# Optimization experiments

Measured on AMD Instinct MI355X. Metric: run time of the kernel, lower is better.

The kernel has to match this reference:

```python
import jax, jax.numpy as jnp
import numpy as np

H = 16          # num_heads
W = 256         # attention_window
D_MODEL = 1024
D_FF = 4096
EPS = 1e-5


def _layernorm(x, g, b):
    mu = jnp.mean(x, axis=-1, keepdims=True)
    var = jnp.mean(jnp.square(x - mu), axis=-1, keepdims=True)
    return (x - mu) * jax.lax.rsqrt(var + EPS) * g + b


def _sliding_attn(q, k, v, w):
    # q,k,v: [B,H,S,d]; each query attends to keys in [i-w, i+w]
    B, Hh, S, d = q.shape
    nc = S // w
    qc = q.reshape(B, Hh, nc, w, d)
    kp = jnp.pad(k, ((0, 0), (0, 0), (w, w), (0, 0)))
    vp = jnp.pad(v, ((0, 0), (0, 0), (w, w), (0, 0)))
    # gather 3w keys per chunk (prev w, current w, next w)
    idx = (jnp.arange(nc) * w)[:, None] + jnp.arange(3 * w)[None, :]  # [nc, 3w]
    kc = kp[:, :, idx, :]  # [B,H,nc,3w,d]
    vc = vp[:, :, idx, :]
    scores = jnp.einsum('bhcqd,bhckd->bhcqk', qc, kc)  # [B,H,nc,w,3w]
    q_pos = jnp.arange(nc)[:, None, None] * w + jnp.arange(w)[None, :, None]
    k_pos = jnp.arange(nc)[:, None, None] * w - w + jnp.arange(3 * w)[None, None, :]
    rel = k_pos - q_pos
    valid = (jnp.abs(rel) <= w) & (k_pos >= 0) & (k_pos < S)  # [nc,w,3w]
    scores = jnp.where(valid[None, None], scores, jnp.float32(-1e9))
    p = jax.nn.softmax(scores, axis=-1)
    out = jnp.einsum('bhcqk,bhckd->bhcqd', p, vc)
    return out.reshape(B, Hh, S, d)


def setup_inputs() -> dict:
    key = jax.random.key(0)
    ks = jax.random.split(key, 8)
    B, S = 2, 4096
    src = jax.random.normal(ks[0], (B, S, D_MODEL), dtype=jnp.float32)
    ln1_g = jnp.ones((D_MODEL,), jnp.float32)
    ln1_b = jnp.zeros((D_MODEL,), jnp.float32)
    ln2_g = jnp.ones((D_MODEL,), jnp.float32)
    ln2_b = jnp.zeros((D_MODEL,), jnp.float32)
    W1 = jax.random.normal(ks[1], (D_MODEL, D_FF), jnp.float32) * 0.02
    b1 = jnp.zeros((D_FF,), jnp.float32)
    W2 = jax.random.normal(ks[2], (D_FF, D_MODEL), jnp.float32) * 0.02
    b2 = jnp.zeros((D_MODEL,), jnp.float32)
    return {"src": src, "ln1_g": ln1_g, "ln1_b": ln1_b, "ln2_g": ln2_g,
            "ln2_b": ln2_b, "W1": W1, "b1": b1, "W2": W2, "b2": b2}


def reference(src, ln1_g, ln1_b, ln2_g, ln2_b, W1, b1, W2, b2):
    B, S, _ = src.shape
    d_head = D_MODEL // H
    qkv = src.reshape(B, S, H, d_head).transpose(0, 2, 1, 3)  # [B,H,S,d]
    attn = _sliding_attn(qkv, qkv, qkv, W)
    attn = attn.transpose(0, 2, 1, 3).reshape(B, S, D_MODEL)
    x = _layernorm(src + attn, ln1_g, ln1_b)
    ff = jnp.maximum(x @ W1 + b1, 0.0) @ W2 + b2
    return _layernorm(x + ff, ln2_g, ln2_b)
```

## Files before the change

### kernel.cpp

```cpp
#include <hip/hip_runtime.h>

typedef __bf16 bf16x8 __attribute__((ext_vector_type(8)));
typedef __bf16 bf16x4 __attribute__((ext_vector_type(4)));
typedef float f32x4 __attribute__((ext_vector_type(4)));

#define MFMA16(a, b, c) __builtin_amdgcn_mfma_f32_16x16x32_bf16((a), (b), (c), 0, 0, 0)

__device__ __forceinline__ void gload_lds16(const void* g, void* l) {
  __builtin_amdgcn_global_load_lds(
      (const __attribute__((address_space(1))) unsigned int*)g,
      (__attribute__((address_space(3))) unsigned int*)l, 16, 0, 0);
}

__global__ __launch_bounds__(256, 2) void attn_kernel(const float* __restrict__ src,
                                                      __bf16* __restrict__ attn_out) {
  const int bid = blockIdx.x;
  const int half = bid & 1;
  const int c = (bid >> 1) & 15;
  const int h = (bid >> 5) & 15;
  const int b = bid >> 9;
  const int tid = threadIdx.x;
  const int w = tid >> 6;
  const int lane = tid & 63;
  const int lg = lane >> 4;
  const int l16 = lane & 15;
  const size_t b4096 = (size_t)b * 4096;

  __shared__ __bf16 Ks[2][64][72];
  __shared__ __bf16 Vt[2][64][72];

  const int q0 = c * 256 + half * 128 + w * 32;
  const float LOG2E = 1.44269504f;

  bf16x8 qf[2][2];
#pragma unroll
  for (int qfi = 0; qfi < 2; ++qfi)
#pragma unroll
    for (int ks = 0; ks < 2; ++ks) {
      const int row = q0 + qfi * 16 + l16;
      const int d0 = ks * 32 + lg * 8;
      const float* p = src + (b4096 + row) * 1024 + h * 64 + d0;
      bf16x8 v;
#pragma unroll
      for (int j = 0; j < 8; ++j) v[j] = (__bf16)(p[j] * LOG2E);
      qf[qfi][ks] = v;
    }

  int krow[4];
#pragma unroll
  for (int kf = 0; kf < 4; ++kf)
    krow[kf] = ((kf >> 1) << 5) + ((l16 >> 2) << 3) + ((kf & 1) << 2) + (l16 & 3);

  const f32x4 z4 = {0.f, 0.f, 0.f, 0.f};
  float m_run[2], l_run[2];
  f32x4 o[2][4];
#pragma unroll
  for (int qfi = 0; qfi < 2; ++qfi) {
    m_run[qfi] = -6.0e8f;
    l_run[qfi] = 0.f;
#pragma unroll
    for (int df = 0; df < 4; ++df) o[qfi][df] = z4;
  }

  const int stage_key = tid >> 2;
  const int d0a = (tid & 3) * 16;
  const int vcolA = stage_key ^ d0a;
  const int vcolB = stage_key ^ (d0a + 8);

  int kpos = c * 256 - 256 + stage_key;
  float4 g4[4];
  {
    const int rc = min(max(kpos, 0), 4095);
    const float* p = src + (b4096 + rc) * 1024 + h * 64 + d0a;
#pragma unroll
    for (int i = 0; i < 4; ++i) g4[i] = *(const float4*)(p + i * 4);
  }

  for (int kt = 0; kt < 12; ++kt) {
    const int kbase = c * 256 - 256 + kt * 64;
    const int cur = kt & 1;
    bf16x8 kvA, kvB;
    const bool inb = ((unsigned)kpos < 4096u);
    kvA[0] = (__bf16)(inb ? g4[0].x : 0.f); kvA[1] = (__bf16)(inb ? g4[0].y : 0.f);
    kvA[2] = (__bf16)(inb ? g4[0].z : 0.f); kvA[3] = (__bf16)(inb ? g4[0].w : 0.f);
    kvA[4] = (__bf16)(inb ? g4[1].x : 0.f); kvA[5] = (__bf16)(inb ? g4[1].y : 0.f);
    kvA[6] = (__bf16)(inb ? g4[1].z : 0.f); kvA[7] = (__bf16)(inb ? g4[1].w : 0.f);
    kvB[0] = (__bf16)(inb ? g4[2].x : 0.f); kvB[1] = (__bf16)(inb ? g4[2].y : 0.f);
    kvB[2] = (__bf16)(inb ? g4[2].z : 0.f); kvB[3] = (__bf16)(inb ? g4[2].w : 0.f);
    kvB[4] = (__bf16)(inb ? g4[3].x : 0.f); kvB[5] = (__bf16)(inb ? g4[3].y : 0.f);
    kvB[6] = (__bf16)(inb ? g4[3].z : 0.f); kvB[7] = (__bf16)(inb ? g4[3].w : 0.f);

    *(bf16x8*)&Ks[cur][stage_key][d0a] = kvA;
    *(bf16x8*)&Ks[cur][stage_key][d0a + 8] = kvB;
#pragma unroll
    for (int j = 0; j < 8; ++j) Vt[cur][d0a + j][vcolA] = kvA[j];
#pragma unroll
    for (int j = 0; j < 8; ++j) Vt[cur][d0a + 8 + j][vcolB] = kvB[j];
    asm volatile("s_waitcnt lgkmcnt(0)" ::: "memory");
    __builtin_amdgcn_s_barrier();
    __builtin_amdgcn_sched_barrier(0);

    kpos += 64;
    if (kt < 11) {
      const int rc = min(max(kpos, 0), 4095);
      const float* p = src + (b4096 + rc) * 1024 + h * 64 + d0a;
#pragma unroll
      for (int i = 0; i < 4; ++i) g4[i] = *(const float4*)(p + i * 4);
    }

    const bool skip = (kbase + 63 < 0) | (kbase >= 4096) |
                      (kbase + 63 < q0 - 256) | (kbase > q0 + 31 + 256);
    if (skip) continue;

    f32x4 s[4][2];
#pragma unroll
    for (int kf = 0; kf < 4; ++kf)
#pragma unroll
      for (int qfi = 0; qfi < 2; ++qfi) s[kf][qfi] = z4;

#pragma unroll
    for (int ks = 0; ks < 2; ++ks) {
      bf16x8 ka[4];
#pragma unroll
      for (int kf = 0; kf < 4; ++kf)
        ka[kf] = *(const bf16x8*)&Ks[cur][krow[kf]][ks * 32 + lg * 8];
#pragma unroll
      for (int kf = 0; kf < 4; ++kf)
#pragma unroll
        for (int qfi = 0; qfi < 2; ++qfi)
          s[kf][qfi] = MFMA16(ka[kf], qf[qfi][ks], s[kf][qfi]);
    }

    const bool needmask = (kbase < 0) | (kbase > 4032) |
                          (kbase < q0 - 225) | (kbase > q0 + 193);
    if (needmask) {
#pragma unroll
      for (int qfi = 0; qfi < 2; ++qfi) {
        const int qp = q0 + qfi * 16 + l16;
#pragma unroll
        for (int kf = 0; kf < 4; ++kf) {
          const int kb0 = kbase + ((kf >> 1) << 5) + 8 * lg + ((kf & 1) << 2);
#pragma unroll
          for (int reg = 0; reg < 4; ++reg) {
            const int kp = kb0 + reg;
            const int rel = kp - qp;
            if (rel > 256 || rel < -256 || kp < 0 || kp >= 4096)
              s[kf][qfi][reg] = -1e9f;
          }
        }
      }
    }

    bf16x4 pb[4][2];
#pragma unroll
    for (int qfi = 0; qfi < 2; ++qfi) {
      float tm = s[0][qfi][0];
#pragma unroll
      for (int kf = 0; kf < 4; ++kf)
#pragma unroll
        for (int reg = 0; reg < 4; ++reg) tm = fmaxf(tm, s[kf][qfi][reg]);
      tm = fmaxf(tm, __shfl_xor(tm, 16, 64));
      tm = fmaxf(tm, __shfl_xor(tm, 32, 64));

      const bool nomax = __all(tm <= m_run[qfi] + 8.f);
      float scl = 1.f;
      if (!nomax) {
        const float mn = fmaxf(m_run[qfi], tm);
        scl = exp2f(m_run[qfi] - mn);
        m_run[qfi] = mn;
#pragma unroll
        for (int df = 0; df < 4; ++df)
#pragma unroll
          for (int reg = 0; reg < 4; ++reg) o[qfi][df][reg] *= scl;
      }
      const float mn = m_run[qfi];

      float rs = 0.f;
#pragma unroll
      for (int kf = 0; kf < 4; ++kf) {
        bf16x4 pv;
#pragma unroll
        for (int reg = 0; reg < 4; ++reg) {
          const float p = exp2f(s[kf][qfi][reg] - mn);
          rs += p;
          pv[reg] = (__bf16)p;
        }
        pb[kf][qfi] = pv;
      }
      rs += __shfl_xor(rs, 16, 64);
      rs += __shfl_xor(rs, 32, 64);
      l_run[qfi] = l_run[qfi] * scl + rs;
    }

#pragma unroll
    for (int ks2 = 0; ks2 < 2; ++ks2) {
      bf16x8 av[4];
#pragma unroll
      for (int df = 0; df < 4; ++df) {
        const int d = df * 16 + l16;
        const int blk = (ks2 * 4 + lg) ^ (d >> 3);
        av[df] = *(const bf16x8*)&Vt[cur][d][blk * 8];
      }
#pragma unroll
      for (int qfi = 0; qfi < 2; ++qfi) {
        const bf16x8 bq = __builtin_shufflevector(pb[2 * ks2][qfi], pb[2 * ks2 + 1][qfi],
                                                  0, 1, 2, 3, 4, 5, 6, 7);
#pragma unroll
        for (int df = 0; df < 4; ++df)
          o[qfi][df] = MFMA16(av[df], bq, o[qfi][df]);
      }
    }
  }

#pragma unroll
  for (int qfi = 0; qfi < 2; ++qfi) {
    const float inv = 1.0f / l_run[qfi];
    const int qp = q0 + qfi * 16 + l16;
    __bf16* dst = attn_out + (b4096 + qp) * 1024 + h * 64 + lg * 4;
#pragma unroll
    for (int df = 0; df < 4; ++df) {
      bf16x4 y;
      y[0] = (__bf16)(o[qfi][df][0] * inv);
      y[1] = (__bf16)(o[qfi][df][1] * inv);
      y[2] = (__bf16)(o[qfi][df][2] * inv);
      y[3] = (__bf16)(o[qfi][df][3] * inv);
      *(bf16x4*)&dst[df * 16] = y;
    }
  }
}

template <int MODE>
__global__ __launch_bounds__(512, 2) void gemm8p(const __bf16* __restrict__ A,
                                                 const __bf16* __restrict__ Bt,
                                                 const float* __restrict__ bias,
                                                 __bf16* __restrict__ out,
                                                 size_t ksplit_stride,
                                                 int M, int N, int Kstride, int Klen) {
  __shared__ char smem[131072];
  const int tid = threadIdx.x;
  const int w = tid >> 6;
  const int lane = tid & 63;
  const int lg = lane >> 4;
  const int l16 = lane & 15;
  const int wr = w >> 2;
  const int wc = w & 3;

  const int nbn = N >> 8;
  const int x = ((int)blockIdx.x & 7) * ((int)gridDim.x >> 3) + ((int)blockIdx.x >> 3);
  const long bm = (long)(x / nbn) * 256;
  const long bn = (long)(x % nbn) * 256;
  const long koff = (long)blockIdx.y * Klen;
  out += (size_t)blockIdx.y * ksplit_stride;

  const f32x4 z4 = {0.f, 0.f, 0.f, 0.f};
  f32x4 acc[8][4];
#pragma unroll
  for (int i = 0; i < 8; ++i)
#pragma unroll
    for (int j = 0; j < 4; ++j) acc[i][j] = z4;

  const int srow = tid >> 2;
  const int g0 = (tid & 3) ^ ((tid >> 3) & 3);
  const __bf16* Ag = A + (size_t)(bm + srow) * Kstride + koff + g0 * 8;
  const __bf16* Bg = Bt + (size_t)(bn + srow) * Kstride + koff + g0 * 8;

  auto stage = [&](int kt, int osel, int isB, int khalf) {
    const __bf16* src = (isB ? Bg : Ag) + (size_t)kt * 64 + khalf * 32;
    char* dst = smem + (isB ? 65536 : 0) + osel * 32768 + khalf * 16384 + (w << 10);
    gload_lds16(src, dst);
    gload_lds16(src + (size_t)128 * Kstride, dst + 8192);
  };

  const int lslot = (lg ^ ((l16 >> 1) & 3)) << 4;
  const char* pA = smem + (wr * 128 + l16) * 64 + lslot;
  const char* pB = smem + 65536 + (wc * 64 + l16) * 64 + lslot;
  auto rdA = [&](int sel, int rf, int ks) {
    return *(const bf16x8*)(pA + sel * 32768 + ks * 16384 + rf * 1024);
  };
  auto rdB = [&](int sel, int cf, int ks) {
    return *(const bf16x8*)(pB + sel * 32768 + ks * 16384 + cf * 1024);
  };

  const int NT = Klen >> 6;

  stage(0, 0, 0, 0);
  stage(0, 0, 1, 0);
  stage(0, 0, 0, 1);
  stage(0, 0, 1, 1);
  asm volatile("s_waitcnt vmcnt(4)" ::: "memory");
  __builtin_amdgcn_s_barrier();
  __builtin_amdgcn_sched_barrier(0);

  for (int t = 0; t < NT; ++t) {
    const int sel = t & 1, osel = sel ^ 1;
    const bool st = (t + 1) < NT;
    bf16x8 af[8], bf[4];

#pragma unroll
    for (int rf = 0; rf < 8; ++rf) af[rf] = rdA(sel, rf, 0);
#pragma unroll
    for (int cf = 0; cf < 4; ++cf) bf[cf] = rdB(sel, cf, 0);
    if (st) { stage(t + 1, osel, 0, 0); stage(t + 1, osel, 1, 0); }
    __builtin_amdgcn_s_setprio(1);
#pragma unroll
    for (int rf = 0; rf < 8; ++rf)
#pragma unroll
      for (int cf = 0; cf < 4; ++cf)
        acc[rf][cf] = MFMA16(af[rf], bf[cf], acc[rf][cf]);
    __builtin_amdgcn_s_setprio(0);
    if (st) asm volatile("s_waitcnt vmcnt(4)" ::: "memory");
    else    asm volatile("s_waitcnt vmcnt(0)" ::: "memory");
    __builtin_amdgcn_s_barrier();
    __builtin_amdgcn_sched_barrier(0);

#pragma unroll
    for (int rf = 0; rf < 8; ++rf) af[rf] = rdA(sel, rf, 1);
#pragma unroll
    for (int cf = 0; cf < 4; ++cf) bf[cf] = rdB(sel, cf, 1);
    if (st) { stage(t + 1, osel, 0, 1); stage(t + 1, osel, 1, 1); }
    __builtin_amdgcn_s_setprio(1);
#pragma unroll
    for (int rf = 0; rf < 8; ++rf)
#pragma unroll
      for (int cf = 0; cf < 4; ++cf)
        acc[rf][cf] = MFMA16(af[rf], bf[cf], acc[rf][cf]);
    __builtin_amdgcn_s_setprio(0);
    if (st) asm volatile("s_waitcnt vmcnt(4)" ::: "memory");
    __builtin_amdgcn_s_barrier();
    __builtin_amdgcn_sched_barrier(0);
  }

  float bv[4];
  if (MODE == 0) {
#pragma unroll
    for (int cf = 0; cf < 4; ++cf) bv[cf] = bias[bn + wc * 64 + cf * 16 + l16];
  }
#pragma unroll
  for (int rf = 0; rf < 8; ++rf)
#pragma unroll
    for (int reg = 0; reg < 4; ++reg) {
      const long row = bm + wr * 128 + rf * 16 + lg * 4 + reg;
#pragma unroll
      for (int cf = 0; cf < 4; ++cf) {
        const long col = bn + wc * 64 + cf * 16 + l16;
        if (MODE == 0) {
          out[row * N + col] = (__bf16)fmaxf(acc[rf][cf][reg] + bv[cf], 0.f);
        } else {
          out[row * N + col] = (__bf16)acc[rf][cf][reg];
        }
      }
    }
}

__global__ __launch_bounds__(256) void transpose_cvt(const float* __restrict__ in,
                                                     __bf16* __restrict__ out,
                                                     int R, int C) {
  __shared__ float tile[64][65];
  const long r0 = (long)blockIdx.y * 64;
  const long c0 = (long)blockIdx.x * 64;
  const int t = threadIdx.x;
  const int tr = t >> 6;
  const int tc = t & 63;
#pragma unroll
  for (int i = 0; i < 16; ++i) {
    const int r = tr * 16 + i;
    tile[r][tc] = in[(r0 + r) * C + c0 + tc];
  }
  __syncthreads();
#pragma unroll
  for (int i = 0; i < 16; ++i) {
    const int cc = tr * 16 + i;
    out[(c0 + cc) * (long)R + r0 + tc] = (__bf16)tile[tc][cc];
  }
}

__global__ __launch_bounds__(256) void ln1_kernel(const float* __restrict__ src,
                                                  const __bf16* __restrict__ attn,
                                                  const float* __restrict__ g,
                                                  const float* __restrict__ bta,
                                                  __bf16* __restrict__ xb) {
  const long r = blockIdx.x;
  const int t = threadIdx.x;
  const float4 a = *(const float4*)&src[r * 1024 + t * 4];
  const bf16x4 cc = *(const bf16x4*)&attn[r * 1024 + t * 4];
  float v[4] = {a.x + (float)cc[0], a.y + (float)cc[1],
                a.z + (float)cc[2], a.w + (float)cc[3]};
  float s = v[0] + v[1] + v[2] + v[3];
  float s2 = v[0] * v[0] + v[1] * v[1] + v[2] * v[2] + v[3] * v[3];
#pragma unroll
  for (int off = 32; off >= 1; off >>= 1) {
    s += __shfl_xor(s, off, 64);
    s2 += __shfl_xor(s2, off, 64);
  }
  __shared__ float red[8];
  if ((t & 63) == 0) { red[t >> 6] = s; red[(t >> 6) + 4] = s2; }
  __syncthreads();
  s = red[0] + red[1] + red[2] + red[3];
  s2 = red[4] + red[5] + red[6] + red[7];
  const float mu = s * (1.f / 1024.f);
  const float var = s2 * (1.f / 1024.f) - mu * mu;
  const float rstd = rsqrtf(var + 1e-5f);
  const float4 gv = *(const float4*)&g[t * 4];
  const float4 bv = *(const float4*)&bta[t * 4];
  bf16x4 y;
  y[0] = (__bf16)((v[0] - mu) * rstd * gv.x + bv.x);
  y[1] = (__bf16)((v[1] - mu) * rstd * gv.y + bv.y);
  y[2] = (__bf16)((v[2] - mu) * rstd * gv.z + bv.z);
  y[3] = (__bf16)((v[3] - mu) * rstd * gv.w + bv.w);
  *(bf16x4*)&xb[r * 1024 + t * 4] = y;
}

__global__ __launch_bounds__(256) void ln2_kernel(const __bf16* __restrict__ xb,
                                                  const __bf16* __restrict__ f0,
                                                  const __bf16* __restrict__ f1,
                                                  const float* __restrict__ b2,
                                                  const float* __restrict__ g,
                                                  const float* __restrict__ bta,
                                                  float* __restrict__ out) {
  const long r = blockIdx.x;
  const int t = threadIdx.x;
  const bf16x4 xv = *(const bf16x4*)&xb[r * 1024 + t * 4];
  const bf16x4 f0v = *(const bf16x4*)&f0[r * 1024 + t * 4];
  const bf16x4 f1v = *(const bf16x4*)&f1[r * 1024 + t * 4];
  const float4 b2v = *(const float4*)&b2[t * 4];
  float v[4];
#pragma unroll
  for (int i = 0; i < 4; ++i)
    v[i] = (float)xv[i] + (float)f0v[i] + (float)f1v[i] +
           ((const float*)&b2v)[i];
  float s = v[0] + v[1] + v[2] + v[3];
  float s2 = v[0] * v[0] + v[1] * v[1] + v[2] * v[2] + v[3] * v[3];
#pragma unroll
  for (int off = 32; off >= 1; off >>= 1) {
    s += __shfl_xor(s, off, 64);
    s2 += __shfl_xor(s2, off, 64);
  }
  __shared__ float red[8];
  if ((t & 63) == 0) { red[t >> 6] = s; red[(t >> 6) + 4] = s2; }
  __syncthreads();
  s = red[0] + red[1] + red[2] + red[3];
  s2 = red[4] + red[5] + red[6] + red[7];
  const float mu = s * (1.f / 1024.f);
  const float var = s2 * (1.f / 1024.f) - mu * mu;
  const float rstd = rsqrtf(var + 1e-5f);
  const float4 gv = *(const float4*)&g[t * 4];
  const float4 bv = *(const float4*)&bta[t * 4];
  float4 y;
  y.x = (v[0] - mu) * rstd * gv.x + bv.x;
  y.y = (v[1] - mu) * rstd * gv.y + bv.y;
  y.z = (v[2] - mu) * rstd * gv.z + bv.z;
  y.w = (v[3] - mu) * rstd * gv.w + bv.w;
  *(float4*)&out[r * 1024 + t * 4] = y;
}

extern "C" void kernel_launch(void* const* d_in, const int* in_sizes, int n_in,
                              void* d_out, int out_size, void* d_ws, size_t ws_size,
                              hipStream_t stream) {
  const float* src = (const float*)d_in[0];
  const float* ln1_g = (const float*)d_in[1];
  const float* ln1_b = (const float*)d_in[2];
  const float* ln2_g = (const float*)d_in[3];
  const float* ln2_b = (const float*)d_in[4];
  const float* W1 = (const float*)d_in[5];
  const float* b1 = (const float*)d_in[6];
  const float* W2 = (const float*)d_in[7];
  const float* b2 = (const float*)d_in[8];
  float* out = (float*)d_out;
  char* ws = (char*)d_ws;

  const size_t MB = 1048576;
  __bf16* xb = (__bf16*)ws;
  __bf16* attn_b = (__bf16*)(ws + 16 * MB);
  __bf16* ffb = attn_b;
  __bf16* ff1b = (__bf16*)(ws + 32 * MB);
  __bf16* w1t = (__bf16*)(ws + 48 * MB);
  __bf16* w2t = (__bf16*)(ws + 56 * MB);
  __bf16* hbuf = (__bf16*)(ws + 64 * MB);

  int Mc = 8192;
  while (Mc > 512 && 64 * MB + (size_t)Mc * 8192 > ws_size) Mc >>= 1;

  transpose_cvt<<<dim3(4096 / 64, 1024 / 64), 256, 0, stream>>>(W1, w1t, 1024, 4096);
  transpose_cvt<<<dim3(1024 / 64, 4096 / 64), 256, 0, stream>>>(W2, w2t, 4096, 1024);
  attn_kernel<<<1024, 256, 0, stream>>>(src, attn_b);
  ln1_kernel<<<8192, 256, 0, stream>>>(src, attn_b, ln1_g, ln1_b, xb);
  for (int m0 = 0; m0 < 8192; m0 += Mc) {
    gemm8p<0><<<dim3((Mc / 256) * (4096 / 256), 1), 512, 0, stream>>>(
        xb + (size_t)m0 * 1024, w1t, b1, hbuf, 0, Mc, 4096, 1024, 1024);
    gemm8p<1><<<dim3((Mc / 256) * (1024 / 256), 2), 512, 0, stream>>>(
        hbuf, w2t, nullptr, ffb + (size_t)m0 * 1024, (size_t)8192 * 1024,
        Mc, 1024, 4096, 2048);
  }
  ln2_kernel<<<8192, 256, 0, stream>>>(xb, ffb, ff1b, b2, ln2_g, ln2_b, out);
}
```

Measured before the change: 242.1 us.

## Triple-buffer K/V LDS staging and overlap next-tile writes with compute

Moves the attention kernel's K/V staging from double to triple LDS buffering. The convert-and-store of tile kt+1 now happens between the QK MFMAs and the softmax/PV of tile kt, with the global load for kt+2 issued two tiles ahead. This leaves one barrier per iteration, and LDS stores and global latency overlap with compute instead of sitting in front of the barrier. In exchange, LDS use grows by half, which may limit occupancy at two blocks per CU, and register pressure rises.

```diff
diff --git a/kernel.cpp b/kernel.cpp
--- a/kernel.cpp
+++ b/kernel.cpp
@@ -11,6 +11,8 @@
       (const __attribute__((address_space(1))) unsigned int*)g,
       (__attribute__((address_space(3))) unsigned int*)l, 16, 0, 0);
 }
+
+struct G4 { float4 a, b, c, d; };
 
 __global__ __launch_bounds__(256, 2) void attn_kernel(const float* __restrict__ src,
                                                       __bf16* __restrict__ attn_out) {
@@ -26,8 +28,8 @@
   const int l16 = lane & 15;
   const size_t b4096 = (size_t)b * 4096;
 
-  __shared__ __bf16 Ks[2][64][72];
-  __shared__ __bf16 Vt[2][64][72];
+  __shared__ __bf16 Ks[3][64][72];
+  __shared__ __bf16 Vt[3][64][72];
 
   const int q0 = c * 256 + half * 128 + w * 32;
   const float LOG2E = 1.44269504f;
@@ -66,51 +68,53 @@
   const int d0a = (tid & 3) * 16;
   const int vcolA = stage_key ^ d0a;
   const int vcolB = stage_key ^ (d0a + 8);
-
-  int kpos = c * 256 - 256 + stage_key;
-  float4 g4[4];
-  {
-    const int rc = min(max(kpos, 0), 4095);
+  const int kb00 = c * 256 - 256;
+
+  auto issue = [&](int n) {
+    const int kp = kb00 + n * 64 + stage_key;
+    const int rc = min(max(kp, 0), 4095);
     const float* p = src + (b4096 + rc) * 1024 + h * 64 + d0a;
-#pragma unroll
-    for (int i = 0; i < 4; ++i) g4[i] = *(const float4*)(p + i * 4);
-  }
+    G4 r;
+    r.a = *(const float4*)(p + 0);
+    r.b = *(const float4*)(p + 4);
+    r.c = *(const float4*)(p + 8);
+    r.d = *(const float4*)(p + 12);
+    return r;
+  };
+  auto cw = [&](int n, const G4& g) {
+    const int kp = kb00 + n * 64 + stage_key;
+    const bool inb = ((unsigned)kp < 4096u);
+    bf16x8 kvA, kvB;
+    kvA[0] = (__bf16)(inb ? g.a.x : 0.f); kvA[1] = (__bf16)(inb ? g.a.y : 0.f);
+    kvA[2] = (__bf16)(inb ? g.a.z : 0.f); kvA[3] = (__bf16)(inb ? g.a.w : 0.f);
+    kvA[4] = (__bf16)(inb ? g.b.x : 0.f); kvA[5] = (__bf16)(inb ? g.b.y : 0.f);
+    kvA[6] = (__bf16)(inb ? g.b.z : 0.f); kvA[7] = (__bf16)(inb ? g.b.w : 0.f);
+    kvB[0] = (__bf16)(inb ? g.c.x : 0.f); kvB[1] = (__bf16)(inb ? g.c.y : 0.f);
+    kvB[2] = (__bf16)(inb ? g.c.z : 0.f); kvB[3] = (__bf16)(inb ? g.c.w : 0.f);
+    kvB[4] = (__bf16)(inb ? g.d.x : 0.f); kvB[5] = (__bf16)(inb ? g.d.y : 0.f);
+    kvB[6] = (__bf16)(inb ? g.d.z : 0.f); kvB[7] = (__bf16)(inb ? g.d.w : 0.f);
+    const int bsel = n % 3;
+    *(bf16x8*)&Ks[bsel][stage_key][d0a] = kvA;
+    *(bf16x8*)&Ks[bsel][stage_key][d0a + 8] = kvB;
+#pragma unroll
+    for (int j = 0; j < 8; ++j) Vt[bsel][d0a + j][vcolA] = kvA[j];
+#pragma unroll
+    for (int j = 0; j < 8; ++j) Vt[bsel][d0a + 8 + j][vcolB] = kvB[j];
+  };
+
+  G4 g = issue(0);
+  cw(0, g);
+  g = issue(1);
+  asm volatile("s_waitcnt lgkmcnt(0)" ::: "memory");
 
   for (int kt = 0; kt < 12; ++kt) {
-    const int kbase = c * 256 - 256 + kt * 64;
-    const int cur = kt & 1;
-    bf16x8 kvA, kvB;
-    const bool inb = ((unsigned)kpos < 4096u);
-    kvA[0] = (__bf16)(inb ? g4[0].x : 0.f); kvA[1] = (__bf16)(inb ? g4[0].y : 0.f);
-    kvA[2] = (__bf16)(inb ? g4[0].z : 0.f); kvA[3] = (__bf16)(inb ? g4[0].w : 0.f);
-    kvA[4] = (__bf16)(inb ? g4[1].x : 0.f); kvA[5] = (__bf16)(inb ? g4[1].y : 0.f);
-    kvA[6] = (__bf16)(inb ? g4[1].z : 0.f); kvA[7] = (__bf16)(inb ? g4[1].w : 0.f);
-    kvB[0] = (__bf16)(inb ? g4[2].x : 0.f); kvB[1] = (__bf16)(inb ? g4[2].y : 0.f);
-    kvB[2] = (__bf16)(inb ? g4[2].z : 0.f); kvB[3] = (__bf16)(inb ? g4[2].w : 0.f);
-    kvB[4] = (__bf16)(inb ? g4[3].x : 0.f); kvB[5] = (__bf16)(inb ? g4[3].y : 0.f);
-    kvB[6] = (__bf16)(inb ? g4[3].z : 0.f); kvB[7] = (__bf16)(inb ? g4[3].w : 0.f);
-
-    *(bf16x8*)&Ks[cur][stage_key][d0a] = kvA;
-    *(bf16x8*)&Ks[cur][stage_key][d0a + 8] = kvB;
-#pragma unroll
-    for (int j = 0; j < 8; ++j) Vt[cur][d0a + j][vcolA] = kvA[j];
-#pragma unroll
-    for (int j = 0; j < 8; ++j) Vt[cur][d0a + 8 + j][vcolB] = kvB[j];
-    asm volatile("s_waitcnt lgkmcnt(0)" ::: "memory");
+    const int kbase = kb00 + kt * 64;
+    const int cur = kt % 3;
     __builtin_amdgcn_s_barrier();
     __builtin_amdgcn_sched_barrier(0);
 
-    kpos += 64;
-    if (kt < 11) {
-      const int rc = min(max(kpos, 0), 4095);
-      const float* p = src + (b4096 + rc) * 1024 + h * 64 + d0a;
-#pragma unroll
-      for (int i = 0; i < 4; ++i) g4[i] = *(const float4*)(p + i * 4);
-    }
-
     const bool skip = (kbase + 63 < 0) | (kbase >= 4096) |
                       (kbase + 63 < q0 - 256) | (kbase > q0 + 31 + 256);
-    if (skip) continue;
 
     f32x4 s[4][2];
 #pragma unroll
@@ -118,98 +122,107 @@
 #pragma unroll
       for (int qfi = 0; qfi < 2; ++qfi) s[kf][qfi] = z4;
 
-#pragma unroll
-    for (int ks = 0; ks < 2; ++ks) {
-      bf16x8 ka[4];
-#pragma unroll
-      for (int kf = 0; kf < 4; ++kf)
-        ka[kf] = *(const bf16x8*)&Ks[cur][krow[kf]][ks * 32 + lg * 8];
-#pragma unroll
-      for (int kf = 0; kf < 4; ++kf)
-#pragma unroll
-        for (int qfi = 0; qfi < 2; ++qfi)
-          s[kf][qfi] = MFMA16(ka[kf], qf[qfi][ks], s[kf][qfi]);
+    if (!skip) {
+#pragma unroll
+      for (int ks = 0; ks < 2; ++ks) {
+        bf16x8 ka[4];
+#pragma unroll
+        for (int kf = 0; kf < 4; ++kf)
+          ka[kf] = *(const bf16x8*)&Ks[cur][krow[kf]][ks * 32 + lg * 8];
+#pragma unroll
+        for (int kf = 0; kf < 4; ++kf)
+#pragma unroll
+          for (int qfi = 0; qfi < 2; ++qfi)
+            s[kf][qfi] = MFMA16(ka[kf], qf[qfi][ks], s[kf][qfi]);
+      }
     }
 
-    const bool needmask = (kbase < 0) | (kbase > 4032) |
-                          (kbase < q0 - 225) | (kbase > q0 + 193);
-    if (needmask) {
-#pragma unroll
-      for (int qfi = 0; qfi < 2; ++qfi) {
-        const int qp = q0 + qfi * 16 + l16;
-#pragma unroll
-        for (int kf = 0; kf < 4; ++kf) {
-          const int kb0 = kbase + ((kf >> 1) << 5) + 8 * lg + ((kf & 1) << 2);
-#pragma unroll
-          for (int reg = 0; reg < 4; ++reg) {
-            const int kp = kb0 + reg;
-            const int rel = kp - qp;
-            if (rel > 256 || rel < -256 || kp < 0 || kp >= 4096)
-              s[kf][qfi][reg] = -1e9f;
+    if (kt + 1 < 12) cw(kt + 1, g);
+    if (kt + 2 < 12) g = issue(kt + 2);
+
+    if (!skip) {
+      const bool needmask = (kbase < 0) | (kbase > 4032) |
+                            (kbase < q0 - 225) | (kbase > q0 + 193);
+      if (needmask) {
+#pragma unroll
+        for (int qfi = 0; qfi < 2; ++qfi) {
+          const int qp = q0 + qfi * 16 + l16;
+#pragma unroll
+          for (int kf = 0; kf < 4; ++kf) {
+            const int kb0 = kbase + ((kf >> 1) << 5) + 8 * lg + ((kf & 1) << 2);
+#pragma unroll
+            for (int reg = 0; reg < 4; ++reg) {
+              const int kp = kb0 + reg;
+              const int rel = kp - qp;
+              if (rel > 256 || rel < -256 || kp < 0 || kp >= 4096)
+                s[kf][qfi][reg] = -1e9f;
+            }
           }
         }
       }
-    }
-
-    bf16x4 pb[4][2];
-#pragma unroll
-    for (int qfi = 0; qfi < 2; ++qfi) {
-      float tm = s[0][qfi][0];
-#pragma unroll
-      for (int kf = 0; kf < 4; ++kf)
-#pragma unroll
-        for (int reg = 0; reg < 4; ++reg) tm = fmaxf(tm, s[kf][qfi][reg]);
-      tm = fmaxf(tm, __shfl_xor(tm, 16, 64));
-      tm = fmaxf(tm, __shfl_xor(tm, 32, 64));
-
-      const bool nomax = __all(tm <= m_run[qfi] + 8.f);
-      float scl = 1.f;
-      if (!nomax) {
-        const float mn = fmaxf(m_run[qfi], tm);
-        scl = exp2f(m_run[qfi] - mn);
-        m_run[qfi] = mn;
-#pragma unroll
-        for (int df = 0; df < 4; ++df)
-#pragma unroll
-          for (int reg = 0; reg < 4; ++reg) o[qfi][df][reg] *= scl;
+
+      bf16x4 pb[4][2];
+#pragma unroll
+      for (int qfi = 0; qfi < 2; ++qfi) {
+        float tm = s[0][qfi][0];
+#pragma unroll
+        for (int kf = 0; kf < 4; ++kf)
+#pragma unroll
+          for (int reg = 0; reg < 4; ++reg) tm = fmaxf(tm, s[kf][qfi][reg]);
+        tm = fmaxf(tm, __shfl_xor(tm, 16, 64));
+        tm = fmaxf(tm, __shfl_xor(tm, 32, 64));
+
+        const bool nomax = __all(tm <= m_run[qfi] + 8.f);
+        float scl = 1.f;
+        if (!nomax) {
+          const float mn = fmaxf(m_run[qfi], tm);
+          scl = exp2f(m_run[qfi] - mn);
+          m_run[qfi] = mn;
+#pragma unroll
+          for (int df = 0; df < 4; ++df)
+#pragma unroll
+            for (int reg = 0; reg < 4; ++reg) o[qfi][df][reg] *= scl;
+        }
+        const float mn = m_run[qfi];
+
+        float rs = 0.f;
+#pragma unroll
+        for (int kf = 0; kf < 4; ++kf) {
+          bf16x4 pv;
+#pragma unroll
+          for (int reg = 0; reg < 4; ++reg) {
+            const float p = exp2f(s[kf][qfi][reg] - mn);
+            rs += p;
+            pv[reg] = (__bf16)p;
+          }
+          pb[kf][qfi] = pv;
+        }
+        rs += __shfl_xor(rs, 16, 64);
+        rs += __shfl_xor(rs, 32, 64);
+        l_run[qfi] = l_run[qfi] * scl + rs;
       }
-      const float mn = m_run[qfi];
-
-      float rs = 0.f;
-#pragma unroll
-      for (int kf = 0; kf < 4; ++kf) {
-        bf16x4 pv;
-#pragma unroll
-        for (int reg = 0; reg < 4; ++reg) {
-          const float p = exp2f(s[kf][qfi][reg] - mn);
-          rs += p;
-          pv[reg] = (__bf16)p;
+
+#pragma unroll
+      for (int ks2 = 0; ks2 < 2; ++ks2) {
+        bf16x8 av[4];
+#pragma unroll
+        for (int df = 0; df < 4; ++df) {
+          const int d = df * 16 + l16;
+          const int blk = (ks2 * 4 + lg) ^ (d >> 3);
+          av[df] = *(const bf16x8*)&Vt[cur][d][blk * 8];
         }
-        pb[kf][qfi] = pv;
-      }
-      rs += __shfl_xor(rs, 16, 64);
-      rs += __shfl_xor(rs, 32, 64);
-      l_run[qfi] = l_run[qfi] * scl + rs;
-    }
-
-#pragma unroll
-    for (int ks2 = 0; ks2 < 2; ++ks2) {
-      bf16x8 av[4];
-#pragma unroll
-      for (int df = 0; df < 4; ++df) {
-        const int d = df * 16 + l16;
-        const int blk = (ks2 * 4 + lg) ^ (d >> 3);
-        av[df] = *(const bf16x8*)&Vt[cur][d][blk * 8];
-      }
-#pragma unroll
-      for (int qfi = 0; qfi < 2; ++qfi) {
-        const bf16x8 bq = __builtin_shufflevector(pb[2 * ks2][qfi], pb[2 * ks2 + 1][qfi],
-                                                  0, 1, 2, 3, 4, 5, 6, 7);
-#pragma unroll
-        for (int df = 0; df < 4; ++df)
-          o[qfi][df] = MFMA16(av[df], bq, o[qfi][df]);
+#pragma unroll
+        for (int qfi = 0; qfi < 2; ++qfi) {
+          const bf16x8 bq = __builtin_shufflevector(pb[2 * ks2][qfi], pb[2 * ks2 + 1][qfi],
+                                                    0, 1, 2, 3, 4, 5, 6, 7);
+#pragma unroll
+          for (int df = 0; df < 4; ++df)
+            o[qfi][df] = MFMA16(av[df], bq, o[qfi][df]);
+        }
       }
     }
+
+    asm volatile("s_waitcnt lgkmcnt(0)" ::: "memory");
   }
 
 #pragma unroll
```

Measured after the change: 244.3 us. Within noise of the previous version (+0.9%).

## Restructure GEMM mainloop into quarter-tile phases with 128-byte swizzled LDS layout

Applied to the files above, without the earlier changes.

Reorganizes the GEMM main loop so each 64-wide K tile is split into four MFMA phases over half-tiles of A and B. Loads for the next tile are issued in quarters interleaved with those phases, so global-to-LDS traffic overlaps compute more finely. The LDS layout moves from two 32-column halves to full 64-column rows of 128 bytes with an XOR swizzle keyed on the row, to avoid bank conflicts. The cost is more barriers per tile and tighter buffer-reuse ordering, which risks races if the stage and barrier sequencing is wrong. It also assumes NT is even.

```diff
diff --git a/kernel.cpp b/kernel.cpp
--- a/kernel.cpp
+++ b/kernel.cpp
@@ -259,75 +259,130 @@
 #pragma unroll
     for (int j = 0; j < 4; ++j) acc[i][j] = z4;
 
-  const int srow = tid >> 2;
-  const int g0 = (tid & 3) ^ ((tid >> 3) & 3);
+  const int srow = tid >> 3;
+  const int g0 = (tid & 7) ^ (srow & 7);
   const __bf16* Ag = A + (size_t)(bm + srow) * Kstride + koff + g0 * 8;
   const __bf16* Bg = Bt + (size_t)(bn + srow) * Kstride + koff + g0 * 8;
-
-  auto stage = [&](int kt, int osel, int isB, int khalf) {
-    const __bf16* src = (isB ? Bg : Ag) + (size_t)kt * 64 + khalf * 32;
-    char* dst = smem + (isB ? 65536 : 0) + osel * 32768 + khalf * 16384 + (w << 10);
-    gload_lds16(src, dst);
-    gload_lds16(src + (size_t)128 * Kstride, dst + 8192);
+  char* ldst = smem + (w << 10);
+
+  auto stage = [&](int kt, int which) {
+    const __bf16* s = ((which & 2) ? Bg : Ag) +
+                      (size_t)((which & 1) * 128) * Kstride + (size_t)kt * 64;
+    char* d = ldst + ((kt & 1) << 16) + ((which & 2) << 14) + ((which & 1) << 14);
+    gload_lds16(s, d);
+    gload_lds16(s + (size_t)64 * Kstride, d + 8192);
   };
 
-  const int lslot = (lg ^ ((l16 >> 1) & 3)) << 4;
-  const char* pA = smem + (wr * 128 + l16) * 64 + lslot;
-  const char* pB = smem + 65536 + (wc * 64 + l16) * 64 + lslot;
+  const unsigned rsw = (unsigned)((l16 & 7) << 4);
+  const char* pA = smem + wr * 16384 + l16 * 128;
+  const char* pB = smem + 32768 + (wc >> 1) * 16384 + ((wc & 1) * 64 + l16) * 128;
   auto rdA = [&](int sel, int rf, int ks) {
-    return *(const bf16x8*)(pA + sel * 32768 + ks * 16384 + rf * 1024);
+    return *(const bf16x8*)(pA + (sel << 16) + rf * 2048 +
+                            ((unsigned)((ks << 6) | (lg << 4)) ^ rsw));
   };
   auto rdB = [&](int sel, int cf, int ks) {
-    return *(const bf16x8*)(pB + sel * 32768 + ks * 16384 + cf * 1024);
+    return *(const bf16x8*)(pB + (sel << 16) + cf * 2048 +
+                            ((unsigned)((ks << 6) | (lg << 4)) ^ rsw));
   };
 
   const int NT = Klen >> 6;
 
-  stage(0, 0, 0, 0);
-  stage(0, 0, 1, 0);
-  stage(0, 0, 0, 1);
-  stage(0, 0, 1, 1);
+  stage(0, 0); stage(0, 1); stage(0, 2); stage(0, 3);
+  stage(1, 2); stage(1, 3);
   asm volatile("s_waitcnt vmcnt(4)" ::: "memory");
   __builtin_amdgcn_s_barrier();
   __builtin_amdgcn_sched_barrier(0);
 
-  for (int t = 0; t < NT; ++t) {
-    const int sel = t & 1, osel = sel ^ 1;
-    const bool st = (t + 1) < NT;
-    bf16x8 af[8], bf[4];
-
-#pragma unroll
-    for (int rf = 0; rf < 8; ++rf) af[rf] = rdA(sel, rf, 0);
-#pragma unroll
-    for (int cf = 0; cf < 4; ++cf) bf[cf] = rdB(sel, cf, 0);
-    if (st) { stage(t + 1, osel, 0, 0); stage(t + 1, osel, 1, 0); }
-    __builtin_amdgcn_s_setprio(1);
-#pragma unroll
-    for (int rf = 0; rf < 8; ++rf)
-#pragma unroll
-      for (int cf = 0; cf < 4; ++cf)
-        acc[rf][cf] = MFMA16(af[rf], bf[cf], acc[rf][cf]);
-    __builtin_amdgcn_s_setprio(0);
-    if (st) asm volatile("s_waitcnt vmcnt(4)" ::: "memory");
-    else    asm volatile("s_waitcnt vmcnt(0)" ::: "memory");
-    __builtin_amdgcn_s_barrier();
-    __builtin_amdgcn_sched_barrier(0);
-
-#pragma unroll
-    for (int rf = 0; rf < 8; ++rf) af[rf] = rdA(sel, rf, 1);
-#pragma unroll
-    for (int cf = 0; cf < 4; ++cf) bf[cf] = rdB(sel, cf, 1);
-    if (st) { stage(t + 1, osel, 0, 1); stage(t + 1, osel, 1, 1); }
-    __builtin_amdgcn_s_setprio(1);
-#pragma unroll
-    for (int rf = 0; rf < 8; ++rf)
-#pragma unroll
-      for (int cf = 0; cf < 4; ++cf)
-        acc[rf][cf] = MFMA16(af[rf], bf[cf], acc[rf][cf]);
-    __builtin_amdgcn_s_setprio(0);
-    if (st) asm volatile("s_waitcnt vmcnt(4)" ::: "memory");
-    __builtin_amdgcn_s_barrier();
-    __builtin_amdgcn_sched_barrier(0);
+  bf16x8 af[4][2], bl[2][2], bh[2][2];
+
+  for (int i = 0; i < (NT >> 1); ++i) {
+    const int a = i << 1;
+    const int b = a + 1, c2 = a + 2, d2 = a + 3;
+    const bool more = (c2 < NT);
+
+#pragma unroll
+    for (int sel = 0; sel < 2; ++sel) {
+      const int tnext = sel ? d2 : c2;
+      const int anext = sel ? c2 : b;
+      const bool stA = sel ? more : true;
+      const bool stB = more;
+
+#pragma unroll
+      for (int rf = 0; rf < 4; ++rf)
+#pragma unroll
+        for (int ks = 0; ks < 2; ++ks) af[rf][ks] = rdA(sel, rf, ks);
+#pragma unroll
+      for (int cf = 0; cf < 2; ++cf)
+#pragma unroll
+        for (int ks = 0; ks < 2; ++ks) bl[cf][ks] = rdB(sel, cf, ks);
+      if (stA) stage(anext, 0);
+      __builtin_amdgcn_s_barrier();
+      asm volatile("s_waitcnt lgkmcnt(0)" ::: "memory");
+      __builtin_amdgcn_sched_barrier(0);
+      __builtin_amdgcn_s_setprio(1);
+#pragma unroll
+      for (int rf = 0; rf < 4; ++rf)
+#pragma unroll
+        for (int cf = 0; cf < 2; ++cf)
+#pragma unroll
+          for (int ks = 0; ks < 2; ++ks)
+            acc[rf][cf] = MFMA16(af[rf][ks], bl[cf][ks], acc[rf][cf]);
+      __builtin_amdgcn_s_setprio(0);
+
+#pragma unroll
+      for (int cf = 0; cf < 2; ++cf)
+#pragma unroll
+        for (int ks = 0; ks < 2; ++ks) bh[cf][ks] = rdB(sel, 2 + cf, ks);
+      if (stA) stage(anext, 1);
+      __builtin_amdgcn_s_barrier();
+      asm volatile("s_waitcnt lgkmcnt(0)" ::: "memory");
+      __builtin_amdgcn_sched_barrier(0);
+      __builtin_amdgcn_s_setprio(1);
+#pragma unroll
+      for (int rf = 0; rf < 4; ++rf)
+#pragma unroll
+        for (int cf = 0; cf < 2; ++cf)
+#pragma unroll
+          for (int ks = 0; ks < 2; ++ks)
+            acc[rf][2 + cf] = MFMA16(af[rf][ks], bh[cf][ks], acc[rf][2 + cf]);
+      __builtin_amdgcn_s_setprio(0);
+
+#pragma unroll
+      for (int rf = 0; rf < 4; ++rf)
+#pragma unroll
+        for (int ks = 0; ks < 2; ++ks) af[rf][ks] = rdA(sel, 4 + rf, ks);
+      if (stB) stage(tnext, 2);
+      __builtin_amdgcn_s_barrier();
+      asm volatile("s_waitcnt lgkmcnt(0)" ::: "memory");
+      __builtin_amdgcn_sched_barrier(0);
+      __builtin_amdgcn_s_setprio(1);
+#pragma unroll
+      for (int rf = 0; rf < 4; ++rf)
+#pragma unroll
+        for (int cf = 0; cf < 2; ++cf)
+#pragma unroll
+          for (int ks = 0; ks < 2; ++ks)
+            acc[4 + rf][cf] = MFMA16(af[rf][ks], bl[cf][ks], acc[4 + rf][cf]);
+      __builtin_amdgcn_s_setprio(0);
+
+      if (stB) {
+        stage(tnext, 3);
+        asm volatile("s_waitcnt vmcnt(4)" ::: "memory");
+      } else {
+        asm volatile("s_waitcnt vmcnt(0)" ::: "memory");
+      }
+      __builtin_amdgcn_s_barrier();
+      __builtin_amdgcn_sched_barrier(0);
+      __builtin_amdgcn_s_setprio(1);
+#pragma unroll
+      for (int rf = 0; rf < 4; ++rf)
+#pragma unroll
+        for (int cf = 0; cf < 2; ++cf)
+#pragma unroll
+          for (int ks = 0; ks < 2; ++ks)
+            acc[4 + rf][2 + cf] = MFMA16(af[rf][ks], bh[cf][ks], acc[4 + rf][2 + cf]);
+      __builtin_amdgcn_s_setprio(0);
+    }
   }
 
   float bv[4];
```

Result: faster. 230.5 us (-4.8%).
